# Performance work log

Hardware: AMD Instinct MI355X
Metric: run time of the kernel (lower is better)

## Reference

```python
import jax, jax.numpy as jnp
from jax import lax
import numpy as np

B, M, LH, K, F, NA, NO = 16, 32, 128, 16, 3, 4, 1


def _conv(x, w, b):
    # x: (B,H,W,Cin), w: (kh,kw,Cin,Cout) -> (B,H,W,Cout), SAME zero padding
    return lax.conv_general_dilated(x, w, (1, 1), 'SAME',
                                    dimension_numbers=('NHWC', 'HWIO', 'NHWC')) + b


def setup_inputs() -> dict:
    key = jax.random.key(0)
    ks = jax.random.split(key, 14)
    s = 0.05
    inp = {
        'map_design': jax.random.uniform(ks[0], (B, NO, M, M), jnp.float32),
        'goal_map':   jax.random.uniform(ks[1], (B, 1, M, M), jnp.float32),
        'W_hid': jax.random.normal(ks[2], (3, 3, NO + 1, LH), jnp.float32) * s,
        'b_hid': jax.random.normal(ks[3], (LH,), jnp.float32) * s,
        'W_h0':  jax.random.normal(ks[4], (3, 3, LH, LH), jnp.float32) * s,
        'b_h0':  jax.random.normal(ks[5], (LH,), jnp.float32) * s,
        'W_c0':  jax.random.normal(ks[6], (3, 3, LH, LH), jnp.float32) * s,
        'b_c0':  jax.random.normal(ks[7], (LH,), jnp.float32) * s,
        'W_f':   jax.random.normal(ks[8], (F, F, LH, 1), jnp.float32) * s,
        'b_f':   jax.random.normal(ks[9], (1,), jnp.float32) * s,
        'W_ih':  jax.random.normal(ks[10], (4 * LH, 1), jnp.float32) * s,
        'b_ih':  jax.random.normal(ks[11], (4 * LH,), jnp.float32) * s,
        'W_hh':  jax.random.normal(ks[12], (4 * LH, LH), jnp.float32) * s,
        'b_hh':  jnp.zeros((4 * LH,), jnp.float32),
        'W_pol': jax.random.normal(ks[13], (LH, NA * NO), jnp.float32) * s,
    }
    return inp


def reference(map_design, goal_map, W_hid, b_hid, W_h0, b_h0, W_c0, b_c0,
              W_f, b_f, W_ih, b_ih, W_hh, b_hh, W_pol):
    # NCHW -> NHWC
    X = jnp.concatenate([map_design, goal_map], axis=1).transpose(0, 2, 3, 1)
    hid = _conv(X, W_hid, b_hid)                      # (B,M,M,LH)
    h0 = _conv(hid, W_h0, b_h0)                       # (B,M,M,LH)
    c0 = _conv(hid, W_c0, b_c0)

    def step(carry, _):
        h, c = carry                                  # (B,M,M,LH)
        inp = _conv(h, W_f, b_f).reshape(-1, 1)       # per-pixel scalar input
        hf = h.reshape(-1, LH)
        gates = inp @ W_ih.T + b_ih + hf @ W_hh.T + b_hh   # (BMM, 4*LH)
        i, f, g, o = jnp.split(gates, 4, axis=-1)     # torch LSTMCell order i,f,g,o
        i, f, o = jax.nn.sigmoid(i), jax.nn.sigmoid(f), jax.nn.sigmoid(o)
        g = jnp.tanh(g)
        c2 = f * c.reshape(-1, LH) + i * g
        h2 = o * jnp.tanh(c2)
        return (h2.reshape(B, M, M, LH), c2.reshape(B, M, M, LH)), None

    (hk, _), _ = lax.scan(step, (h0, c0), None, length=K - 1)

    # policy: 1x1 conv == per-pixel matmul
    logits_hw = jnp.einsum('bhwc,ca->bhwa', hk, W_pol)     # (B,M,M,NA*NO)
    logits = logits_hw.transpose(0, 3, 1, 2)               # (B,NA*NO,M,M)
    probs = jax.nn.softmax(logits.reshape(B * NO, NA, M, M), axis=1)
    logits = logits.reshape(B, NO, NA, M, M).transpose(0, 2, 1, 3, 4)
    probs = probs.reshape(B, NO, NA, M, M).transpose(0, 2, 1, 3, 4)
    return logits, probs
```

## Files before the change

### kernel.cpp

```cpp
#include <hip/hip_runtime.h>

#define MM 32
#define LH 128
#define NSTEPS 15
#define SSTR 136
#define NBLK 256
#define FSTR 32
#define SIDX(row,pxi,ch) (((row)*34 + (pxi))*SSTR + (ch))

typedef __bf16  bf16x8  __attribute__((ext_vector_type(8)));
typedef float   floatx4 __attribute__((ext_vector_type(4)));
typedef unsigned long long ull;

#define L2E 1.4426950408889634f

__device__ __forceinline__ float ex2(float x){
#if __has_builtin(__builtin_amdgcn_exp2f)
  return __builtin_amdgcn_exp2f(x);
#else
  float r; asm volatile("v_exp_f32 %0, %1\n\ts_nop 0" : "=v"(r) : "v"(x)); return r;
#endif
}
__device__ __forceinline__ float frcp(float x){ return __builtin_amdgcn_rcpf(x); }

__device__ __forceinline__ unsigned short cvt_bf16(float x){
  __bf16 b = (__bf16)x; unsigned short u; __builtin_memcpy(&u, &b, 2); return u;
}
__device__ __forceinline__ float bf2f(unsigned short u){
  union { unsigned u2; float f; } v; v.u2 = ((unsigned)u) << 16;
  return v.f;
}

__device__ __forceinline__ void st_dev(ull* p, ull v){
  __hip_atomic_store(p, v, __ATOMIC_RELAXED, __HIP_MEMORY_SCOPE_AGENT);
}
__device__ __forceinline__ ull ld_dev(ull* p){
  return __hip_atomic_load(p, __ATOMIC_RELAXED, __HIP_MEMORY_SCOPE_AGENT);
}
__device__ __forceinline__ void wait_flag(int* f, int target){
  while ((int)(__hip_atomic_load(f, __ATOMIC_RELAXED, __HIP_MEMORY_SCOPE_AGENT) - target) < 0){
    __builtin_amdgcn_s_sleep(1);
  }
}
__device__ __forceinline__ void set_flag(int* f, int v){
  __hip_atomic_store(f, v, __ATOMIC_RELAXED, __HIP_MEMORY_SCOPE_AGENT);
}

__global__ __launch_bounds__(512, 2) void k_mega(
    const float* __restrict__ mp,   const float* __restrict__ gl,
    const float* __restrict__ W_hid,const float* __restrict__ b_hid,
    const float* __restrict__ W_h0, const float* __restrict__ b_h0,
    const float* __restrict__ W_c0, const float* __restrict__ b_c0,
    const float* __restrict__ Wf,   const float* __restrict__ bfs,
    const float* __restrict__ wih,  const float* __restrict__ bih,
    const float* __restrict__ Whh,  const float* __restrict__ bhh,
    const float* __restrict__ wpol,
    unsigned short* __restrict__ wc0, unsigned short* __restrict__ wc1,
    unsigned short* __restrict__ whhf, float* __restrict__ bsum,
    unsigned short* __restrict__ wfbF,
    ull* __restrict__ expbuf,
    int* __restrict__ flags, float* __restrict__ out)
{
  __shared__ __attribute__((aligned(16))) unsigned short sH[4*34*SSTR];
  __shared__ float sCv[6][3][36];
  __shared__ float sOwn[2][2][32];
  __shared__ float sImp[2][32];

  int t = threadIdx.x, blk = blockIdx.x;
  int pair = blk & 15, b = blk >> 4;
  int y0 = pair*2;
  int wave = t >> 6, l = t & 63, m16 = l & 15, quad = l >> 4;
  bool hasU = (pair > 0), hasD = (pair < 15);
  int ch = wave*16 + m16;

  for (int c = blk*512 + t; c < 91904; c += NBLK*512){
    if (c < 73728){
      int which = (c >= 36864) ? 1 : 0;
      int cc = which ? c - 36864 : c;
      int i2 = cc*4, frag = i2 >> 9, rem = i2 & 511, ll = rem >> 3, e0 = rem & 7;
      int kk = frag >> 5, ct = (frag >> 2) & 7, kc = frag & 3;
      int co = ct*16 + (ll & 15), ci0 = kc*32 + ((ll >> 4) << 3) + e0;
      const float* src = which ? W_c0 : W_h0;
      ull v = 0;
      #pragma unroll
      for (int j=0;j<4;j++) v |= (ull)cvt_bf16(src[(kk<<14) + (ci0+j)*128 + co]) << (16*j);
      st_dev((ull*)(which ? wc1 : wc0) + cc, v);
    } else if (c < 90112){
      int cc = c - 73728;
      int i2 = cc*4, frag = i2 >> 9, rem = i2 & 511, ll = rem >> 3, e0 = rem & 7;
      int q = frag >> 5, ct = (frag >> 2) & 7, kc = frag & 3;
      float scq = (q == 2) ? (2.f*L2E) : (-L2E);
      int rw = q*128 + ct*16 + (ll & 15), col = kc*32 + ((ll >> 4) << 3) + e0;
      const float* s4 = Whh + rw*128 + col;
      ull v = 0;
      #pragma unroll
      for (int j=0;j<4;j++) v |= (ull)cvt_bf16(s4[j]*scq) << (16*j);
      st_dev((ull*)whhf + cc, v);
    } else if (c < 90368){
      int cc = c - 90112; int j = cc*2;
      union { float f[2]; ull u; } pv;
      pv.f[0] = bih[j] + bhh[j]; pv.f[1] = bih[j+1] + bhh[j+1];
      st_dev((ull*)bsum + cc, pv.u);
    } else {
      int cc = c - 90368;
      int i2 = cc*4, frag = i2 >> 9, rem = i2 & 511, ll = rem >> 3, e0 = rem & 7;
      int ky = frag >> 2, kc = frag & 3;
      int n = ll & 15, k0 = kc*32 + ((ll >> 4) << 3) + e0;
      ull v = 0;
      if (n < 3){
        #pragma unroll
        for (int j=0;j<4;j++) v |= (ull)cvt_bf16(Wf[(ky*3 + n)*128 + k0 + j]) << (16*j);
      }
      st_dev((ull*)wfbF + cc, v);
    }
  }
  if (t < 128){
    int p = t >> 6, w2 = t & 63;
    st_dev(expbuf + ((size_t)p*NBLK + blk)*64 + w2, 0);
  }
  __syncthreads();
  if (t == 0) set_flag(&flags[blk*FSTR], 1);

  {
    int hch = t & 127, g = t >> 7;
    float wz0[9], wz1[9];
    #pragma unroll
    for (int kk=0;kk<9;kk++){ wz0[kk] = W_hid[(kk*2)*LH + hch];
                              wz1[kk] = W_hid[(kk*2+1)*LH + hch]; }
    float bh = b_hid[hch];
    int yi = y0 - 1 + g;
    bool valid = (yi >= 0 && yi < MM);
    for (int x = 0; x < MM; x++){
      float acc2 = 0.f;
      if (valid){
        acc2 = bh;
        #pragma unroll
        for (int ky=0; ky<3; ky++){
          int yy = yi + ky - 1; if (yy < 0 || yy >= MM) continue;
          #pragma unroll
          for (int kx=0; kx<3; kx++){
            int xx = x + kx - 1; if (xx < 0 || xx >= MM) continue;
            int gi = (b*MM + yy)*MM + xx;
            acc2 += mp[gi]*wz0[ky*3+kx] + gl[gi]*wz1[ky*3+kx];
          }
        }
      }
      sH[SIDX(g, x+1, hch)] = cvt_bf16(acc2);
    }
  }
  if (t < 256){
    int k = t >> 6, col = ((t >> 5) & 1) ? 33 : 0, c4 = t & 31;
    *(ull*)&sH[SIDX(k, col, c4*4)] = 0;
  }
  if (t < 6){ sCv[t][0][32] = 0.f; sCv[t][2][1] = 0.f; }
  if (t < 180) wait_flag(&flags[t*FSTR], 1);
  __syncthreads();

  float c_reg[4][4];
  {
    floatx4 acch[4], accc[4];
    #pragma unroll
    for (int mt=0;mt<4;mt++){ acch[mt] = (floatx4){0.f,0.f,0.f,0.f};
                              accc[mt] = (floatx4){0.f,0.f,0.f,0.f}; }
    #pragma unroll
    for (int kk=0; kk<9; kk++){
      int ky = kk/3, kx = kk%3;
      #pragma unroll
      for (int kc=0; kc<4; kc++){
        int frag = ((kk*8 + wave)*4 + kc);
        bf16x8 b0 = *(const bf16x8*)(wc0 + (frag << 9) + l*8);
        bf16x8 b1 = *(const bf16x8*)(wc1 + (frag << 9) + l*8);
        #pragma unroll
        for (int mt=0; mt<4; mt++){
          bf16x8 a = *(const bf16x8*)&sH[SIDX((mt>>1)+ky, m16 + (mt&1)*16 + kx, kc*32 + quad*8)];
          acch[mt] = __builtin_amdgcn_mfma_f32_16x16x32_bf16(a, b0, acch[mt], 0,0,0);
          accc[mt] = __builtin_amdgcn_mfma_f32_16x16x32_bf16(a, b1, accc[mt], 0,0,0);
        }
      }
    }
    __syncthreads();
    float bh = b_h0[ch], bc = b_c0[ch];
    #pragma unroll
    for (int mt=0; mt<4; mt++)
      #pragma unroll
      for (int r=0; r<4; r++){
        int px = mt*16 + quad*4 + r;
        c_reg[mt][r] = accc[mt][r] + bc;
        sH[SIDX(1+(px>>5), (px&31)+1, ch)] = cvt_bf16(acch[mt][r] + bh);
      }
  }
  __syncthreads();

  bf16x8 bfr[4][4];
  #pragma unroll
  for (int q=0;q<4;q++)
    #pragma unroll
    for (int kc=0;kc<4;kc++)
      bfr[q][kc] = *(const bf16x8*)(whhf + (((q*32 + wave*4 + kc) << 9)) + l*8);

  int ri = wave & 1, rky = wave >> 1;
  bf16x8 wfC[4];
  if (wave < 6){
    #pragma unroll
    for (int kc=0;kc<4;kc++)
      wfC[kc] = *(const bf16x8*)(wfbF + (((rky*4 + kc) << 9) + l*8));
  }
  float wv[4], bs[4];
  #pragma unroll
  for (int q=0;q<4;q++){
    float scq = (q == 2) ? (2.f*L2E) : (-L2E);
    int g = q*128 + ch;
    wv[q] = wih[g]*scq; bs[q] = bsum[g]*scq;
  }
  float bf0 = bfs[0];

  for (int s = 0; s < NSTEPS; s++){
    int cur = s & 1;

    if (wave < 6){
      bool isExp = (wave == 1) || (wave == 4);
      bool doit = !isExp || (wave == 1 ? hasD : hasU);
      if (doit){
        if (isExp) __builtin_amdgcn_s_setprio(1);
        floatx4 p0 = (floatx4){0.f,0.f,0.f,0.f};
        floatx4 p1 = (floatx4){0.f,0.f,0.f,0.f};
        #pragma unroll
        for (int kc=0;kc<4;kc++){
          bf16x8 aL = *(const bf16x8*)&sH[SIDX(1+ri, m16 + 1,  kc*32 + quad*8)];
          bf16x8 aR = *(const bf16x8*)&sH[SIDX(1+ri, m16 + 17, kc*32 + quad*8)];
          p0 = __builtin_amdgcn_mfma_f32_16x16x32_bf16(aL, wfC[kc], p0, 0,0,0);
          p1 = __builtin_amdgcn_mfma_f32_16x16x32_bf16(aR, wfC[kc], p1, 0,0,0);
        }
        if (m16 < 3){
          #pragma unroll
          for (int r=0;r<4;r++){
            sCv[wave][m16][quad*4 + r + m16]      = p0[r];
            sCv[wave][m16][16 + quad*4 + r + m16] = p1[r];
          }
        }
        __asm__ __volatile__("" ::: "memory");
        if (l < 32){
          float v = sCv[wave][0][l+1] + sCv[wave][1][l+1] + sCv[wave][2][l+1];
          if (wave == 1 || wave == 4){
            union { float f; unsigned u; } pv; pv.f = v;
            ull pk = ((ull)(unsigned)(2 + s) << 32) | (ull)pv.u;
            st_dev(expbuf + ((size_t)cur*NBLK + blk)*64 + (wave == 1 ? 32 : 0) + l, pk);
          } else if (wave == 0){
            sOwn[1][0][l] = bf0 + v;
          } else if (wave == 2){
            sOwn[0][0][l] = bf0 + v;
          } else if (wave == 3){
            sOwn[1][1][l] = v;
          } else {
            sOwn[0][1][l] = v;
          }
        }
        if (isExp) __builtin_amdgcn_s_setprio(0);
      }
    }

    floatx4 acc[4][4];
    #pragma unroll
    for (int mt=0;mt<4;mt++)
      #pragma unroll
      for (int q=0;q<4;q++) acc[mt][q] = (floatx4){0.f,0.f,0.f,0.f};
    #pragma unroll
    for (int kc=0; kc<4; kc++){
      bf16x8 a[4];
      #pragma unroll
      for (int mt=0;mt<4;mt++)
        a[mt] = *(const bf16x8*)&sH[SIDX(1+(mt>>1), m16 + (mt&1)*16 + 1, kc*32 + quad*8)];
      #pragma unroll
      for (int q=0; q<4; q++)
        #pragma unroll
        for (int mt=0; mt<4; mt++)
          acc[mt][q] = __builtin_amdgcn_mfma_f32_16x16x32_bf16(a[mt], bfr[q][kc], acc[mt][q], 0,0,0);
    }

    if (wave == 7){
      int d = l >> 5, x = l & 31;
      bool ok = d ? hasD : hasU;
      float v = 0.f;
      if (ok){
        ull* p = expbuf + ((size_t)cur*NBLK + (d ? blk+1 : blk-1))*64 + (d ? 0 : 32) + x;
        unsigned tgt = (unsigned)(2 + s);
        ull c0 = ld_dev(p);
        ull c1 = ld_dev(p);
        while ((int)((unsigned)(c0 >> 32) - tgt) < 0){
          c0 = c1;
          c1 = ld_dev(p);
        }
        union { unsigned u; float f; } pv; pv.u = (unsigned)c0; v = pv.f;
      }
      sImp[d][x] = v;
    }
    __syncthreads();

    #pragma unroll
    for (int mt=0; mt<4; mt++){
      int row = mt >> 1;
      #pragma unroll
      for (int r=0; r<4; r++){
        int x = ((mt & 1) << 4) + quad*4 + r;
        float iv = sOwn[row][0][x] + sOwn[row][1][x] + sImp[row][x];
        float p0 = acc[mt][0][r] + iv*wv[0] + bs[0];
        float p1 = acc[mt][1][r] + iv*wv[1] + bs[1];
        float p2 = acc[mt][2][r] + iv*wv[2] + bs[2];
        float p3 = acc[mt][3][r] + iv*wv[3] + bs[3];
        float ig = frcp(1.f + ex2(p0));
        float fg = frcp(1.f + ex2(p1));
        float gg = 1.f - 2.f*frcp(1.f + ex2(p2));
        float og = frcp(1.f + ex2(p3));
        float cn = fg*c_reg[mt][r] + ig*gg;
        c_reg[mt][r] = cn;
        float th = 1.f - 2.f*frcp(1.f + ex2((2.f*L2E)*cn));
        sH[SIDX(1+row, x+1, ch)] = cvt_bf16(og*th);
      }
    }
    __syncthreads();
  }

  {
    int px = t >> 3, s8 = t & 7;
    int base = SIDX(1+(px>>5), (px&31)+1, s8*16);
    uint4 h0v = *(const uint4*)&sH[base];
    uint4 h1v = *(const uint4*)&sH[base + 8];
    float la[4] = {0.f,0.f,0.f,0.f};
    const unsigned short* hu = (const unsigned short*)&h0v;
    #pragma unroll
    for (int e=0;e<8;e++){
      int c = s8*16 + e; float hv2 = bf2f(hu[e]);
      const float* w4 = wpol + c*4;
      la[0]+=hv2*w4[0]; la[1]+=hv2*w4[1]; la[2]+=hv2*w4[2]; la[3]+=hv2*w4[3];
    }
    hu = (const unsigned short*)&h1v;
    #pragma unroll
    for (int e=0;e<8;e++){
      int c = s8*16 + 8 + e; float hv2 = bf2f(hu[e]);
      const float* w4 = wpol + c*4;
      la[0]+=hv2*w4[0]; la[1]+=hv2*w4[1]; la[2]+=hv2*w4[2]; la[3]+=hv2*w4[3];
    }
    #pragma unroll
    for (int a=0;a<4;a++){
      la[a] += __shfl_xor(la[a], 1, 64);
      la[a] += __shfl_xor(la[a], 2, 64);
      la[a] += __shfl_xor(la[a], 4, 64);
    }
    if (s8 == 0){
      int y = y0 + (px>>5), x = px & 31;
      float m = fmaxf(fmaxf(la[0],la[1]),fmaxf(la[2],la[3]));
      float e[4]; float sum = 0.f;
      #pragma unroll
      for (int a=0;a<4;a++){ e[a]=__expf(la[a]-m); sum+=e[a]; }
      float inv = frcp(sum);
      #pragma unroll
      for (int a=0;a<4;a++){
        int o = ((b*4 + a)*MM + y)*MM + x;
        out[o] = la[a];
        out[65536 + o] = e[a]*inv;
      }
    }
  }
}

extern "C" void kernel_launch(void* const* d_in, const int* in_sizes, int n_in,
                              void* d_out, int out_size, void* d_ws, size_t ws_size,
                              hipStream_t stream){
  const float* mp    = (const float*)d_in[0];
  const float* gl    = (const float*)d_in[1];
  const float* W_hid = (const float*)d_in[2];
  const float* b_hid = (const float*)d_in[3];
  const float* W_h0  = (const float*)d_in[4];
  const float* b_h0  = (const float*)d_in[5];
  const float* W_c0  = (const float*)d_in[6];
  const float* b_c0  = (const float*)d_in[7];
  const float* W_f   = (const float*)d_in[8];
  const float* b_f   = (const float*)d_in[9];
  const float* W_ih  = (const float*)d_in[10];
  const float* b_ih  = (const float*)d_in[11];
  const float* W_hh  = (const float*)d_in[12];
  const float* b_hh  = (const float*)d_in[13];
  const float* W_pol = (const float*)d_in[14];
  float* out = (float*)d_out;

  char* ws = (char*)d_ws;
  unsigned short* whhf  = (unsigned short*)ws;
  float*          bsum  = (float*)(ws + (128<<10));
  unsigned short* wc0   = (unsigned short*)(ws + (132<<10));
  unsigned short* wc1   = (unsigned short*)(ws + (420<<10));
  unsigned short* wfbF  = (unsigned short*)(ws + (708<<10));
  int*            flags = (int*)(ws + (720<<10));
  ull*            expbuf= (ull*)(ws + (784<<10));

  k_mega<<<NBLK, 512, 0, stream>>>(
      mp, gl, W_hid, b_hid, W_h0, b_h0, W_c0, b_c0, W_f, b_f,
      W_ih, b_ih, W_hh, b_hh, W_pol,
      wc0, wc1, whhf, bsum, wfbF, expbuf, flags, out);
}
```

Measured before the change: 170.3 us.

## Add fast-path halo exchange via workgroup-scope stores and remap block-to-row layout

Block indices are remapped so vertically adjacent row-pairs sit 8 blocks apart, likely so neighbours land on the same XCD and share an L2. Halo values are now written twice: once with workgroup-scope relaxed stores to a second buffer, read with sc0 loads that hit the shared L2, and once with agent-scope stores as before. An adaptive budgeted poll tries the fast buffer first and falls back to the device-coherent buffer after repeated misses. The goal is lower cross-block handoff latency per step. The cost is an extra store per value, and correctness depends on the assumed block-to-XCD placement, which the fallback guards against.

```diff
diff --git a/kernel.cpp b/kernel.cpp
--- a/kernel.cpp
+++ b/kernel.cpp
@@ -36,6 +36,15 @@
 }
 __device__ __forceinline__ ull ld_dev(ull* p){
   return __hip_atomic_load(p, __ATOMIC_RELAXED, __HIP_MEMORY_SCOPE_AGENT);
+}
+__device__ __forceinline__ void st_wg(ull* p, ull v){
+  __hip_atomic_store(p, v, __ATOMIC_RELAXED, __HIP_MEMORY_SCOPE_WORKGROUP);
+}
+__device__ __forceinline__ ull ld_sc0(ull* p){
+  ull v;
+  asm volatile("global_load_dwordx2 %0, %1, off sc0\n\ts_waitcnt vmcnt(0)"
+               : "=v"(v) : "v"((ull)p) : "memory");
+  return v;
 }
 __device__ __forceinline__ void wait_flag(int* f, int target){
   while ((int)(__hip_atomic_load(f, __ATOMIC_RELAXED, __HIP_MEMORY_SCOPE_AGENT) - target) < 0){
@@ -58,7 +67,7 @@
     unsigned short* __restrict__ wc0, unsigned short* __restrict__ wc1,
     unsigned short* __restrict__ whhf, float* __restrict__ bsum,
     unsigned short* __restrict__ wfbF,
-    ull* __restrict__ expbuf,
+    ull* __restrict__ expA, ull* __restrict__ expF,
     int* __restrict__ flags, float* __restrict__ out)
 {
   __shared__ __attribute__((aligned(16))) unsigned short sH[4*34*SSTR];
@@ -67,8 +76,10 @@
   __shared__ float sImp[2][32];
 
   int t = threadIdx.x, blk = blockIdx.x;
-  int pair = blk & 15, b = blk >> 4;
+  int pair = (blk >> 3) & 15;
+  int b = (blk & 7) | ((blk >> 7) << 3);
   int y0 = pair*2;
+  int nU = blk - 8, nD = blk + 8;
   int wave = t >> 6, l = t & 63, m16 = l & 15, quad = l >> 4;
   bool hasU = (pair > 0), hasD = (pair < 15);
   int ch = wave*16 + m16;
@@ -116,7 +127,8 @@
   }
   if (t < 128){
     int p = t >> 6, w2 = t & 63;
-    st_dev(expbuf + ((size_t)p*NBLK + blk)*64 + w2, 0);
+    st_dev(expA + ((size_t)p*NBLK + blk)*64 + w2, 0);
+    st_wg (expF + ((size_t)p*NBLK + blk)*64 + w2, 0);
   }
   __syncthreads();
   if (t == 0) set_flag(&flags[blk*FSTR], 1);
@@ -213,6 +225,7 @@
     wv[q] = wih[g]*scq; bs[q] = bsum[g]*scq;
   }
   float bf0 = bfs[0];
+  int fmode = 0, fails = 0;
 
   for (int s = 0; s < NSTEPS; s++){
     int cur = s & 1;
@@ -244,7 +257,9 @@
           if (wave == 1 || wave == 4){
             union { float f; unsigned u; } pv; pv.f = v;
             ull pk = ((ull)(unsigned)(2 + s) << 32) | (ull)pv.u;
-            st_dev(expbuf + ((size_t)cur*NBLK + blk)*64 + (wave == 1 ? 32 : 0) + l, pk);
+            size_t idx = ((size_t)cur*NBLK + blk)*64 + (wave == 1 ? 32 : 0) + l;
+            st_wg (expF + idx, pk);
+            st_dev(expA + idx, pk);
           } else if (wave == 0){
             sOwn[1][0][l] = bf0 + v;
           } else if (wave == 2){
@@ -282,15 +297,26 @@
       bool ok = d ? hasD : hasU;
       float v = 0.f;
       if (ok){
-        ull* p = expbuf + ((size_t)cur*NBLK + (d ? blk+1 : blk-1))*64 + (d ? 0 : 32) + x;
+        size_t idx = ((size_t)cur*NBLK + (d ? nD : nU))*64 + (d ? 0 : 32) + x;
         unsigned tgt = (unsigned)(2 + s);
-        ull c0 = ld_dev(p);
-        ull c1 = ld_dev(p);
-        while ((int)((unsigned)(c0 >> 32) - tgt) < 0){
-          c0 = c1;
-          c1 = ld_dev(p);
-        }
-        union { unsigned u; float f; } pv; pv.u = (unsigned)c0; v = pv.f;
+        ull val = 0; bool got = false;
+        if (fmode != 2){
+          int budget = (fmode == 1) ? 64 : 24;
+          for (int i = 0; i < budget; i++){
+            ull vv = ld_sc0(expF + idx);
+            if ((int)((unsigned)(vv >> 32) - tgt) >= 0){ val = vv; got = true; break; }
+          }
+          if (got){ fmode = 1; fails = 0; }
+          else if (fmode == 1){ fmode = 0; fails = 1; }
+          else if (++fails >= 3){ fmode = 2; }
+        }
+        if (!got){
+          ull* p = expA + idx;
+          ull c0 = ld_dev(p), c1 = ld_dev(p);
+          while ((int)((unsigned)(c0 >> 32) - tgt) < 0){ c0 = c1; c1 = ld_dev(p); }
+          val = c0;
+        }
+        union { unsigned u; float f; } pv; pv.u = (unsigned)val; v = pv.f;
       }
       sImp[d][x] = v;
     }
@@ -390,10 +416,11 @@
   unsigned short* wc1   = (unsigned short*)(ws + (420<<10));
   unsigned short* wfbF  = (unsigned short*)(ws + (708<<10));
   int*            flags = (int*)(ws + (720<<10));
-  ull*            expbuf= (ull*)(ws + (784<<10));
+  ull*            expA  = (ull*)(ws + (784<<10));
+  ull*            expF  = (ull*)(ws + (1040<<10));
 
   k_mega<<<NBLK, 512, 0, stream>>>(
       mp, gl, W_hid, b_hid, W_h0, b_h0, W_c0, b_c0, W_f, b_f,
       W_ih, b_ih, W_hh, b_hh, W_pol,
-      wc0, wc1, whhf, bsum, wfbF, expbuf, flags, out);
-}
+      wc0, wc1, whhf, bsum, wfbF, expA, expF, flags, out);
+}
```

After: 182.5 us. +7.2%, slower.

## Keep halo rows locally and recompute them to hide neighbor exchange latency

Applied to the files above, without the earlier changes.

Each block now stores and computes LSTM state for its two own rows plus one halo row above and below. This lets it first update interior rows using its own conv inputs, then update the halo rows, while the neighbor's exchanged scalar is fetched speculatively and waited on later. W_hh and Wf fragments are no longer held in registers but reloaded from global memory each step, which frees registers (launch bounds no longer request 2 blocks per CU). The cost is doubled recurrent matmul work per block, more LDS, and extra global weight traffic per step.

```diff
diff --git a/kernel.cpp b/kernel.cpp
--- a/kernel.cpp
+++ b/kernel.cpp
@@ -46,7 +46,7 @@
   __hip_atomic_store(f, v, __ATOMIC_RELAXED, __HIP_MEMORY_SCOPE_AGENT);
 }
 
-__global__ __launch_bounds__(512, 2) void k_mega(
+__global__ __launch_bounds__(512) void k_mega(
     const float* __restrict__ mp,   const float* __restrict__ gl,
     const float* __restrict__ W_hid,const float* __restrict__ b_hid,
     const float* __restrict__ W_h0, const float* __restrict__ b_h0,
@@ -61,14 +61,15 @@
     ull* __restrict__ expbuf,
     int* __restrict__ flags, float* __restrict__ out)
 {
-  __shared__ __attribute__((aligned(16))) unsigned short sH[4*34*SSTR];
-  __shared__ float sCv[6][3][36];
-  __shared__ float sOwn[2][2][32];
+  __shared__ __attribute__((aligned(16))) unsigned short sH[6*34*SSTR];
+  __shared__ float sCv[10][3][36];
+  __shared__ float sOwn[4][3][32];
   __shared__ float sImp[2][32];
 
   int t = threadIdx.x, blk = blockIdx.x;
   int pair = blk & 15, b = blk >> 4;
   int y0 = pair*2;
+  int nU = blk - 1, nD = blk + 1;
   int wave = t >> 6, l = t & 63, m16 = l & 15, quad = l >> 4;
   bool hasU = (pair > 0), hasD = (pair < 15);
   int ch = wave*16 + m16;
@@ -128,39 +129,41 @@
     for (int kk=0;kk<9;kk++){ wz0[kk] = W_hid[(kk*2)*LH + hch];
                               wz1[kk] = W_hid[(kk*2+1)*LH + hch]; }
     float bh = b_hid[hch];
-    int yi = y0 - 1 + g;
-    bool valid = (yi >= 0 && yi < MM);
-    for (int x = 0; x < MM; x++){
-      float acc2 = 0.f;
-      if (valid){
-        acc2 = bh;
-        #pragma unroll
-        for (int ky=0; ky<3; ky++){
-          int yy = yi + ky - 1; if (yy < 0 || yy >= MM) continue;
+    for (int rr = g; rr < 6; rr += 4){
+      int yi = y0 - 2 + rr;
+      bool valid = (yi >= 0 && yi < MM);
+      for (int x = 0; x < MM; x++){
+        float acc2 = 0.f;
+        if (valid){
+          acc2 = bh;
           #pragma unroll
-          for (int kx=0; kx<3; kx++){
-            int xx = x + kx - 1; if (xx < 0 || xx >= MM) continue;
-            int gi = (b*MM + yy)*MM + xx;
-            acc2 += mp[gi]*wz0[ky*3+kx] + gl[gi]*wz1[ky*3+kx];
+          for (int ky=0; ky<3; ky++){
+            int yy = yi + ky - 1; if (yy < 0 || yy >= MM) continue;
+            #pragma unroll
+            for (int kx=0; kx<3; kx++){
+              int xx = x + kx - 1; if (xx < 0 || xx >= MM) continue;
+              int gi = (b*MM + yy)*MM + xx;
+              acc2 += mp[gi]*wz0[ky*3+kx] + gl[gi]*wz1[ky*3+kx];
+            }
           }
         }
-      }
-      sH[SIDX(g, x+1, hch)] = cvt_bf16(acc2);
-    }
-  }
-  if (t < 256){
+        sH[SIDX(rr, x+1, hch)] = cvt_bf16(acc2);
+      }
+    }
+  }
+  if (t < 384){
     int k = t >> 6, col = ((t >> 5) & 1) ? 33 : 0, c4 = t & 31;
     *(ull*)&sH[SIDX(k, col, c4*4)] = 0;
   }
-  if (t < 6){ sCv[t][0][32] = 0.f; sCv[t][2][1] = 0.f; }
+  if (t < 10){ sCv[t][0][32] = 0.f; sCv[t][2][1] = 0.f; }
   if (t < 180) wait_flag(&flags[t*FSTR], 1);
   __syncthreads();
 
-  float c_reg[4][4];
+  float c_reg[8][4];
   {
-    floatx4 acch[4], accc[4];
-    #pragma unroll
-    for (int mt=0;mt<4;mt++){ acch[mt] = (floatx4){0.f,0.f,0.f,0.f};
+    floatx4 acch[8], accc[8];
+    #pragma unroll
+    for (int mt=0;mt<8;mt++){ acch[mt] = (floatx4){0.f,0.f,0.f,0.f};
                               accc[mt] = (floatx4){0.f,0.f,0.f,0.f}; }
     #pragma unroll
     for (int kk=0; kk<9; kk++){
@@ -171,7 +174,7 @@
         bf16x8 b0 = *(const bf16x8*)(wc0 + (frag << 9) + l*8);
         bf16x8 b1 = *(const bf16x8*)(wc1 + (frag << 9) + l*8);
         #pragma unroll
-        for (int mt=0; mt<4; mt++){
+        for (int mt=0; mt<8; mt++){
           bf16x8 a = *(const bf16x8*)&sH[SIDX((mt>>1)+ky, m16 + (mt&1)*16 + kx, kc*32 + quad*8)];
           acch[mt] = __builtin_amdgcn_mfma_f32_16x16x32_bf16(a, b0, acch[mt], 0,0,0);
           accc[mt] = __builtin_amdgcn_mfma_f32_16x16x32_bf16(a, b1, accc[mt], 0,0,0);
@@ -181,30 +184,19 @@
     __syncthreads();
     float bh = b_h0[ch], bc = b_c0[ch];
     #pragma unroll
-    for (int mt=0; mt<4; mt++)
+    for (int mt=0; mt<8; mt++){
+      bool dead = (mt < 2 && !hasU) || (mt >= 6 && !hasD);
       #pragma unroll
       for (int r=0; r<4; r++){
-        int px = mt*16 + quad*4 + r;
-        c_reg[mt][r] = accc[mt][r] + bc;
-        sH[SIDX(1+(px>>5), (px&31)+1, ch)] = cvt_bf16(acch[mt][r] + bh);
-      }
+        int x = (mt&1)*16 + quad*4 + r;
+        float hv = dead ? 0.f : (acch[mt][r] + bh);
+        c_reg[mt][r] = dead ? 0.f : (accc[mt][r] + bc);
+        sH[SIDX(1+(mt>>1), x+1, ch)] = cvt_bf16(hv);
+      }
+    }
   }
   __syncthreads();
 
-  bf16x8 bfr[4][4];
-  #pragma unroll
-  for (int q=0;q<4;q++)
-    #pragma unroll
-    for (int kc=0;kc<4;kc++)
-      bfr[q][kc] = *(const bf16x8*)(whhf + (((q*32 + wave*4 + kc) << 9)) + l*8);
-
-  int ri = wave & 1, rky = wave >> 1;
-  bf16x8 wfC[4];
-  if (wave < 6){
-    #pragma unroll
-    for (int kc=0;kc<4;kc++)
-      wfC[kc] = *(const bf16x8*)(wfbF + (((rky*4 + kc) << 9) + l*8));
-  }
   float wv[4], bs[4];
   #pragma unroll
   for (int q=0;q<4;q++){
@@ -216,97 +208,100 @@
 
   for (int s = 0; s < NSTEPS; s++){
     int cur = s & 1;
-
-    if (wave < 6){
-      bool isExp = (wave == 1) || (wave == 4);
-      bool doit = !isExp || (wave == 1 ? hasD : hasU);
-      if (doit){
-        if (isExp) __builtin_amdgcn_s_setprio(1);
-        floatx4 p0 = (floatx4){0.f,0.f,0.f,0.f};
-        floatx4 p1 = (floatx4){0.f,0.f,0.f,0.f};
+    unsigned tgt = (unsigned)(2 + s);
+
+    ull specv = 0; ull* pP = nullptr;
+    if (wave == 5 && hasU && l < 32){
+      pP = expbuf + ((size_t)cur*NBLK + nU)*64 + 32 + l;
+      specv = ld_dev(pP);
+    } else if (wave == 6 && hasD && l < 32){
+      pP = expbuf + ((size_t)cur*NBLK + nD)*64 + l;
+      specv = ld_dev(pP);
+    }
+
+    if (wave < 5){
+      int d0, d1;
+      switch (wave){
+        case 0:  d0 = 1|(1<<2)|(1<<4)|(1<<6);         d1 = 2|(1<<2)|(2<<4)|(1<<6); break;
+        case 1:  d0 = 1|(0<<2)|(2<<4)|(0<<6)|(2<<8);  d1 = 0|(0<<2)|(1<<4)|(0<<6); break;
+        case 2:  d0 = 2|(2<<2)|(1<<4)|(2<<6)|(1<<8);  d1 = 3|(2<<2)|(2<<4)|(2<<6); break;
+        case 3:  d0 = 0|(1<<2)|(0<<4)|(1<<6);         d1 = 1|(2<<2)|(0<<4)|(2<<6); break;
+        default: d0 = 2|(0<<2)|(3<<4)|(0<<6);         d1 = 3|(1<<2)|(3<<4)|(1<<6); break;
+      }
+      #pragma unroll
+      for (int wp = 0; wp < 2; wp++){
+        int dsc = wp ? d1 : d0;
+        int R = dsc & 3, ky = (dsc>>2)&3, dR = (dsc>>4)&3, dP = (dsc>>6)&3, pub = (dsc>>8)&3;
+        int slot = wave*2 + wp;
+        floatx4 q0 = (floatx4){0.f,0.f,0.f,0.f};
+        floatx4 q1 = (floatx4){0.f,0.f,0.f,0.f};
         #pragma unroll
         for (int kc=0;kc<4;kc++){
-          bf16x8 aL = *(const bf16x8*)&sH[SIDX(1+ri, m16 + 1,  kc*32 + quad*8)];
-          bf16x8 aR = *(const bf16x8*)&sH[SIDX(1+ri, m16 + 17, kc*32 + quad*8)];
-          p0 = __builtin_amdgcn_mfma_f32_16x16x32_bf16(aL, wfC[kc], p0, 0,0,0);
-          p1 = __builtin_amdgcn_mfma_f32_16x16x32_bf16(aR, wfC[kc], p1, 0,0,0);
+          bf16x8 wf = *(const bf16x8*)(wfbF + (((ky*4 + kc) << 9) + l*8));
+          bf16x8 aL = *(const bf16x8*)&sH[SIDX(1+R, m16 + 1,  kc*32 + quad*8)];
+          bf16x8 aR = *(const bf16x8*)&sH[SIDX(1+R, m16 + 17, kc*32 + quad*8)];
+          q0 = __builtin_amdgcn_mfma_f32_16x16x32_bf16(aL, wf, q0, 0,0,0);
+          q1 = __builtin_amdgcn_mfma_f32_16x16x32_bf16(aR, wf, q1, 0,0,0);
         }
         if (m16 < 3){
           #pragma unroll
           for (int r=0;r<4;r++){
-            sCv[wave][m16][quad*4 + r + m16]      = p0[r];
-            sCv[wave][m16][16 + quad*4 + r + m16] = p1[r];
+            sCv[slot][m16][quad*4 + r + m16]      = q0[r];
+            sCv[slot][m16][16 + quad*4 + r + m16] = q1[r];
           }
         }
         __asm__ __volatile__("" ::: "memory");
         if (l < 32){
-          float v = sCv[wave][0][l+1] + sCv[wave][1][l+1] + sCv[wave][2][l+1];
-          if (wave == 1 || wave == 4){
-            union { float f; unsigned u; } pv; pv.f = v;
-            ull pk = ((ull)(unsigned)(2 + s) << 32) | (ull)pv.u;
-            st_dev(expbuf + ((size_t)cur*NBLK + blk)*64 + (wave == 1 ? 32 : 0) + l, pk);
-          } else if (wave == 0){
-            sOwn[1][0][l] = bf0 + v;
-          } else if (wave == 2){
-            sOwn[0][0][l] = bf0 + v;
-          } else if (wave == 3){
-            sOwn[1][1][l] = v;
-          } else {
-            sOwn[0][1][l] = v;
+          float v = sCv[slot][0][l+1] + sCv[slot][1][l+1] + sCv[slot][2][l+1];
+          if (pub){
+            bool okp = (pub == 2) ? hasD : hasU;
+            if (okp){
+              union { float f; unsigned u; } pv; pv.f = v;
+              st_dev(expbuf + ((size_t)cur*NBLK + blk)*64 + ((pub == 2) ? 32 : 0) + l,
+                     ((ull)tgt << 32) | (ull)pv.u);
+            }
           }
-        }
-        if (isExp) __builtin_amdgcn_s_setprio(0);
-      }
-    }
-
-    floatx4 acc[4][4];
-    #pragma unroll
-    for (int mt=0;mt<4;mt++)
-      #pragma unroll
-      for (int q=0;q<4;q++) acc[mt][q] = (floatx4){0.f,0.f,0.f,0.f};
+          sOwn[dR][dP][l] = v;
+        }
+      }
+    }
+
+    ull wa = (ull)whhf;
+    asm volatile("" : "+v"(wa));
+    const unsigned short* wp8 = (const unsigned short*)wa;
+    floatx4 accO[4][4];
+    #pragma unroll
+    for (int m=0;m<4;m++)
+      #pragma unroll
+      for (int q=0;q<4;q++) accO[m][q] = (floatx4){0.f,0.f,0.f,0.f};
     #pragma unroll
     for (int kc=0; kc<4; kc++){
-      bf16x8 a[4];
-      #pragma unroll
-      for (int mt=0;mt<4;mt++)
-        a[mt] = *(const bf16x8*)&sH[SIDX(1+(mt>>1), m16 + (mt&1)*16 + 1, kc*32 + quad*8)];
-      #pragma unroll
-      for (int q=0; q<4; q++)
-        #pragma unroll
-        for (int mt=0; mt<4; mt++)
-          acc[mt][q] = __builtin_amdgcn_mfma_f32_16x16x32_bf16(a[mt], bfr[q][kc], acc[mt][q], 0,0,0);
-    }
-
-    if (wave == 7){
-      int d = l >> 5, x = l & 31;
-      bool ok = d ? hasD : hasU;
-      float v = 0.f;
-      if (ok){
-        ull* p = expbuf + ((size_t)cur*NBLK + (d ? blk+1 : blk-1))*64 + (d ? 0 : 32) + x;
-        unsigned tgt = (unsigned)(2 + s);
-        ull c0 = ld_dev(p);
-        ull c1 = ld_dev(p);
-        while ((int)((unsigned)(c0 >> 32) - tgt) < 0){
-          c0 = c1;
-          c1 = ld_dev(p);
-        }
-        union { unsigned u; float f; } pv; pv.u = (unsigned)c0; v = pv.f;
-      }
-      sImp[d][x] = v;
+      bf16x8 a0 = *(const bf16x8*)&sH[SIDX(2, m16 + 1,  kc*32 + quad*8)];
+      bf16x8 a1 = *(const bf16x8*)&sH[SIDX(2, m16 + 17, kc*32 + quad*8)];
+      bf16x8 a2 = *(const bf16x8*)&sH[SIDX(3, m16 + 1,  kc*32 + quad*8)];
+      bf16x8 a3 = *(const bf16x8*)&sH[SIDX(3, m16 + 17, kc*32 + quad*8)];
+      #pragma unroll
+      for (int q=0; q<4; q++){
+        bf16x8 bq = *(const bf16x8*)(wp8 + ((q*32 + wave*4 + kc) << 9) + l*8);
+        accO[0][q] = __builtin_amdgcn_mfma_f32_16x16x32_bf16(a0, bq, accO[0][q], 0,0,0);
+        accO[1][q] = __builtin_amdgcn_mfma_f32_16x16x32_bf16(a1, bq, accO[1][q], 0,0,0);
+        accO[2][q] = __builtin_amdgcn_mfma_f32_16x16x32_bf16(a2, bq, accO[2][q], 0,0,0);
+        accO[3][q] = __builtin_amdgcn_mfma_f32_16x16x32_bf16(a3, bq, accO[3][q], 0,0,0);
+      }
     }
     __syncthreads();
 
     #pragma unroll
-    for (int mt=0; mt<4; mt++){
-      int row = mt >> 1;
+    for (int m=0; m<4; m++){
+      int mt = 2 + m, rw = 1 + (m>>1);
       #pragma unroll
       for (int r=0; r<4; r++){
-        int x = ((mt & 1) << 4) + quad*4 + r;
-        float iv = sOwn[row][0][x] + sOwn[row][1][x] + sImp[row][x];
-        float p0 = acc[mt][0][r] + iv*wv[0] + bs[0];
-        float p1 = acc[mt][1][r] + iv*wv[1] + bs[1];
-        float p2 = acc[mt][2][r] + iv*wv[2] + bs[2];
-        float p3 = acc[mt][3][r] + iv*wv[3] + bs[3];
+        int x = (m&1)*16 + quad*4 + r;
+        float iv = ((bf0 + sOwn[rw][0][x]) + sOwn[rw][1][x]) + sOwn[rw][2][x];
+        float p0 = accO[m][0][r] + iv*wv[0] + bs[0];
+        float p1 = accO[m][1][r] + iv*wv[1] + bs[1];
+        float p2 = accO[m][2][r] + iv*wv[2] + bs[2];
+        float p3 = accO[m][3][r] + iv*wv[3] + bs[3];
         float ig = frcp(1.f + ex2(p0));
         float fg = frcp(1.f + ex2(p1));
         float gg = 1.f - 2.f*frcp(1.f + ex2(p2));
@@ -314,7 +309,68 @@
         float cn = fg*c_reg[mt][r] + ig*gg;
         c_reg[mt][r] = cn;
         float th = 1.f - 2.f*frcp(1.f + ex2((2.f*L2E)*cn));
-        sH[SIDX(1+row, x+1, ch)] = cvt_bf16(og*th);
+        sH[SIDX(1+rw, x+1, ch)] = cvt_bf16(og*th);
+      }
+    }
+
+    floatx4 accH[4][4];
+    #pragma unroll
+    for (int m=0;m<4;m++)
+      #pragma unroll
+      for (int q=0;q<4;q++) accH[m][q] = (floatx4){0.f,0.f,0.f,0.f};
+    #pragma unroll
+    for (int kc=0; kc<4; kc++){
+      bf16x8 a0 = *(const bf16x8*)&sH[SIDX(1, m16 + 1,  kc*32 + quad*8)];
+      bf16x8 a1 = *(const bf16x8*)&sH[SIDX(1, m16 + 17, kc*32 + quad*8)];
+      bf16x8 a2 = *(const bf16x8*)&sH[SIDX(4, m16 + 1,  kc*32 + quad*8)];
+      bf16x8 a3 = *(const bf16x8*)&sH[SIDX(4, m16 + 17, kc*32 + quad*8)];
+      #pragma unroll
+      for (int q=0; q<4; q++){
+        bf16x8 bq = *(const bf16x8*)(wp8 + ((q*32 + wave*4 + kc) << 9) + l*8);
+        accH[0][q] = __builtin_amdgcn_mfma_f32_16x16x32_bf16(a0, bq, accH[0][q], 0,0,0);
+        accH[1][q] = __builtin_amdgcn_mfma_f32_16x16x32_bf16(a1, bq, accH[1][q], 0,0,0);
+        accH[2][q] = __builtin_amdgcn_mfma_f32_16x16x32_bf16(a2, bq, accH[2][q], 0,0,0);
+        accH[3][q] = __builtin_amdgcn_mfma_f32_16x16x32_bf16(a3, bq, accH[3][q], 0,0,0);
+      }
+    }
+
+    if (pP){
+      ull val = specv;
+      if ((int)((unsigned)(val >> 32) - tgt) < 0){
+        ull c0 = ld_dev(pP), c1 = ld_dev(pP);
+        while ((int)((unsigned)(c0 >> 32) - tgt) < 0){ c0 = c1; c1 = ld_dev(pP); }
+        val = c0;
+      }
+      union { unsigned u; float f; } pv; pv.u = (unsigned)val;
+      sImp[(wave == 5) ? 0 : 1][l] = pv.f;
+    }
+    __syncthreads();
+
+    #pragma unroll
+    for (int m=0; m<4; m++){
+      int mt = (m < 2) ? m : (4 + m);
+      int rw = (m < 2) ? 0 : 3;
+      if ((rw == 0) ? hasU : hasD){
+        #pragma unroll
+        for (int r=0; r<4; r++){
+          int x = (m&1)*16 + quad*4 + r;
+          float pa = (rw == 0) ? sImp[0][x] : sOwn[3][0][x];
+          float pc = sOwn[rw][1][x];
+          float pb = (rw == 0) ? sOwn[0][2][x] : sImp[1][x];
+          float iv = ((bf0 + pa) + pc) + pb;
+          float p0 = accH[m][0][r] + iv*wv[0] + bs[0];
+          float p1 = accH[m][1][r] + iv*wv[1] + bs[1];
+          float p2 = accH[m][2][r] + iv*wv[2] + bs[2];
+          float p3 = accH[m][3][r] + iv*wv[3] + bs[3];
+          float ig = frcp(1.f + ex2(p0));
+          float fg = frcp(1.f + ex2(p1));
+          float gg = 1.f - 2.f*frcp(1.f + ex2(p2));
+          float og = frcp(1.f + ex2(p3));
+          float cn = fg*c_reg[mt][r] + ig*gg;
+          c_reg[mt][r] = cn;
+          float th = 1.f - 2.f*frcp(1.f + ex2((2.f*L2E)*cn));
+          sH[SIDX((rw == 0) ? 1 : 4, x+1, ch)] = cvt_bf16(og*th);
+        }
       }
     }
     __syncthreads();
@@ -322,7 +378,7 @@
 
   {
     int px = t >> 3, s8 = t & 7;
-    int base = SIDX(1+(px>>5), (px&31)+1, s8*16);
+    int base = SIDX(2+(px>>5), (px&31)+1, s8*16);
     uint4 h0v = *(const uint4*)&sH[base];
     uint4 h1v = *(const uint4*)&sH[base + 8];
     float la[4] = {0.f,0.f,0.f,0.f};
```

Result: slower. 313.2 us (+83.9%).
